# Performance work log

Hardware: AMD Instinct MI355X
Metric: run time of the kernel (lower is better)

The kernel has to match this reference:

```python
import math
import jax, jax.numpy as jnp
import numpy as np

B, T, D = 2, 2048, 2048
DH, NQ, NKV = 128, 16, 4
QPG = NQ // NKV  # queries per group = 4
ROPE_BASE = 10000.0
YARN_SCALE = 2.0
ORIG_MAX_LEN = 4096
BETA_FAST, BETA_SLOW = 32.0, 1.0
EPS = 1.1920929e-07  # torch.finfo(float32).eps, RMSNorm default
MSCALE = 0.1 * math.log(YARN_SCALE) + 1.0
ATTN_SCALE = 1.0 / (MSCALE * math.sqrt(DH))


def _yarn_inv_freq():
    inv_freq = 1.0 / ROPE_BASE ** (np.arange(0, DH, 2, dtype=np.float32) / DH)
    wavelengths = 2.0 * math.pi / inv_freq
    low_w = ORIG_MAX_LEN / BETA_SLOW
    high_w = ORIG_MAX_LEN / BETA_FAST
    gamma = np.clip((low_w - wavelengths) / (low_w - high_w), 0.0, 1.0)
    return (gamma * inv_freq + (1.0 - gamma) * inv_freq / YARN_SCALE).astype(np.float32)


def setup_inputs() -> dict:
    key = jax.random.key(0)
    k0, k1, k2, k3 = jax.random.split(key, 4)
    x = jax.random.normal(k0, (B, T, D), jnp.float32)
    Wq = jax.random.normal(k1, (D, DH * NQ), jnp.float32) * 0.02
    Wkv = jax.random.normal(k2, (D, 2 * DH * NKV), jnp.float32) * 0.02
    Wout = jax.random.normal(k3, (DH * NQ, D), jnp.float32) * 0.02
    q_norm_w = jnp.ones((DH,), jnp.float32)
    k_norm_w = jnp.ones((DH,), jnp.float32)
    inv_freq = jnp.asarray(_yarn_inv_freq())
    return {"x": x, "Wq": Wq, "Wkv": Wkv, "Wout": Wout,
            "q_norm_w": q_norm_w, "k_norm_w": k_norm_w, "inv_freq": inv_freq}


def _rmsnorm(x, w):
    ms = jnp.mean(jnp.square(x), axis=-1, keepdims=True)
    return x * jax.lax.rsqrt(ms + EPS) * w


def _apply_rope(x, inv_freq):
    # x: (..., T, DH)
    t = jnp.arange(x.shape[-2], dtype=inv_freq.dtype)
    freqs = jnp.outer(t, inv_freq)               # (T, DH//2)
    emb = jnp.concatenate([freqs, freqs], -1)     # (T, DH)
    cos, sin = jnp.cos(emb), jnp.sin(emb)
    half = x.shape[-1] // 2
    x_rot = jnp.concatenate([-x[..., half:], x[..., :half]], -1)
    return x * cos + x_rot * sin


def reference(x, Wq, Wkv, Wout, q_norm_w, k_norm_w, inv_freq):
    q = x @ Wq                                    # (B, T, NQ*DH)
    kv = x @ Wkv                                  # (B, T, 2*NKV*DH)
    k, v = jnp.split(kv, 2, axis=-1)              # each (B, T, NKV*DH)
    # b t (qpg g d) -> b qpg g t d
    q = q.reshape(B, T, QPG, NKV, DH).transpose(0, 2, 3, 1, 4)
    # b t (g d) -> b g t d
    k = k.reshape(B, T, NKV, DH).transpose(0, 2, 1, 3)
    v = v.reshape(B, T, NKV, DH).transpose(0, 2, 1, 3)
    q = _apply_rope(_rmsnorm(q, q_norm_w), inv_freq)
    k = _apply_rope(_rmsnorm(k, k_norm_w), inv_freq)
    scores = jnp.einsum('bqgtd,bgsd->bqgts', q, k) * ATTN_SCALE
    causal = jnp.tril(jnp.ones((T, T), bool))
    scores = jnp.where(causal, scores, -jnp.inf)
    attn = jax.nn.softmax(scores, axis=-1)
    out = jnp.einsum('bqgts,bgsd->bqgtd', attn, v)
    # b qpg g t d -> b t (qpg g d)
    out = out.transpose(0, 3, 1, 2, 4).reshape(B, T, NQ * DH)
    return out @ Wout
```

## Files before the change

kernel.cpp:

```cpp
#include <hip/hip_runtime.h>
#include <math.h>


typedef __attribute__((ext_vector_type(8))) short s16x8;
typedef __attribute__((ext_vector_type(4))) float f32x4;
typedef __attribute__((ext_vector_type(4))) unsigned int u32x4;

__device__ __forceinline__ unsigned short f2bf(float x) {
  union { float f; unsigned int u; } v; v.f = x;
  return (unsigned short)((v.u + 0x7FFFu + ((v.u >> 16) & 1u)) >> 16);
}

__device__ __forceinline__ float bf2f(unsigned short x) {
  union { unsigned int u; float f; } v; v.u = (unsigned int)x << 16;
  return v.f;
}

__device__ __forceinline__ unsigned int cvt_pk_bf16(float lo, float hi) {
  unsigned int r;
  asm("v_cvt_pk_bf16_f32 %0, %1, %2" : "=v"(r) : "v"(lo), "v"(hi));
  return r;
}

#define GLD_LDS16(g, l)                                            \
  __builtin_amdgcn_global_load_lds(                                \
      (const __attribute__((address_space(1))) void*)(g),          \
      (__attribute__((address_space(3))) void*)(l), 16, 0, 0)

__device__ __forceinline__ void wtrans_body(const float* __restrict__ in,
                                            unsigned short* __restrict__ out,
                                            int R, int C, int bx, int by,
                                            unsigned short lt[64][65]) {
  const int r0 = bx * 64, c0 = by * 64;
  const int j = threadIdx.x & 63, i4 = threadIdx.x >> 6;
#pragma unroll
  for (int p = 0; p < 16; ++p) {
    int i = p * 4 + i4;
    lt[i][j] = f2bf(in[(size_t)(r0 + i) * C + c0 + j]);
  }
  __syncthreads();
#pragma unroll
  for (int p = 0; p < 16; ++p) {
    int i = p * 4 + i4;
    out[(size_t)(c0 + i) * R + r0 + j] = lt[j][i];
  }
}

__global__ __launch_bounds__(256) void prep1_k(const float* __restrict__ x,
                                               const float* __restrict__ Wq,
                                               const float* __restrict__ Wkv,
                                               const float* __restrict__ Wout,
                                               const float* __restrict__ invf,
                                               unsigned short* __restrict__ xb,
                                               unsigned short* __restrict__ wqkvt,
                                               unsigned short* __restrict__ wot,
                                               float2* __restrict__ cstab) {
  __shared__ unsigned short lt[64][65];
  const int bid = blockIdx.x;
  if (bid < 8192) {
    int i = bid * 256 + threadIdx.x;
    float4 v = ((const float4*)x)[i];
    unsigned long long pack = (unsigned long long)f2bf(v.x)
                            | ((unsigned long long)f2bf(v.y) << 16)
                            | ((unsigned long long)f2bf(v.z) << 32)
                            | ((unsigned long long)f2bf(v.w) << 48);
    ((unsigned long long*)xb)[i] = pack;
  } else if (bid < 9216) {
    int b2 = bid - 8192;
    wtrans_body(Wq, wqkvt, 2048, 2048, b2 & 31, b2 >> 5, lt);
  } else if (bid < 9728) {
    int b2 = bid - 9216;
    wtrans_body(Wkv, wqkvt + (size_t)2048 * 2048, 2048, 1024, b2 & 31, b2 >> 5, lt);
  } else if (bid < 10752) {
    int b2 = bid - 9728;
    wtrans_body(Wout, wot, 2048, 2048, b2 & 31, b2 >> 5, lt);
  } else {
    int i = (bid - 10752) * 256 + threadIdx.x;
    int t = i >> 6, f = i & 63;
    float s, c;
    sincosf((float)t * invf[f], &s, &c);
    cstab[i] = make_float2(c, s);
  }
}

template <int OUTBF>
__global__ __launch_bounds__(256) void gemm_bt_t(const unsigned short* __restrict__ A,
                                                 const unsigned short* __restrict__ Bt,
                                                 void* __restrict__ Cv,
                                                 int M, int N, int K) {
  __shared__ alignas(16) unsigned short sA[2][128][32];
  __shared__ alignas(16) unsigned short sB[2][128][32];
  const int tid = threadIdx.x;
  const int lane = tid & 63;
  const int w = tid >> 6;
  const int wm = (w >> 1) * 64, wn = (w & 1) * 64;
  const int nwg = gridDim.x * gridDim.y;
  int bid = blockIdx.y * gridDim.x + blockIdx.x;
  bid = (bid & 7) * (nwg >> 3) + (bid >> 3);
  const int m0 = (bid % gridDim.x) * 128, n0 = (bid / gridDim.x) * 128;
  const int l15 = lane & 15, lhi = lane >> 4;
  f32x4 acc[4][4];
#pragma unroll
  for (int i = 0; i < 4; ++i)
#pragma unroll
    for (int j = 0; j < 4; ++j) acc[i][j] = (f32x4){0.f, 0.f, 0.f, 0.f};
  const int row = tid >> 2;
  const int srcslot = (tid & 3) ^ ((row >> 1) & 3);
  const unsigned short* gA0 = A + (size_t)(m0 + row) * K + srcslot * 8;
  const unsigned short* gA1 = A + (size_t)(m0 + 64 + row) * K + srcslot * 8;
  const unsigned short* gB0 = Bt + (size_t)(n0 + row) * K + srcslot * 8;
  const unsigned short* gB1 = Bt + (size_t)(n0 + 64 + row) * K + srcslot * 8;
  char* ldsA = (char*)&sA[0][0][0] + w * 1024;
  char* ldsB = (char*)&sB[0][0][0] + w * 1024;
  auto STAGE = [&](int bb, int k0) {
    GLD_LDS16(gA0 + k0, ldsA + bb * 8192);
    GLD_LDS16(gA1 + k0, ldsA + bb * 8192 + 4096);
    GLD_LDS16(gB0 + k0, ldsB + bb * 8192);
    GLD_LDS16(gB1 + k0, ldsB + bb * 8192 + 4096);
  };
  const int sphys = (lhi ^ ((l15 >> 1) & 3)) * 8;
  const int nt = K >> 5;
  STAGE(0, 0);
  __syncthreads();
  int cur = 0;
  for (int t = 0; t < nt; ++t) {
    if (t + 1 < nt) STAGE(cur ^ 1, (t + 1) * 32);
    s16x8 af[4], bfr[4];
#pragma unroll
    for (int i = 0; i < 4; ++i) af[i] = *(const s16x8*)&sA[cur][wm + i * 16 + l15][sphys];
#pragma unroll
    for (int j = 0; j < 4; ++j) bfr[j] = *(const s16x8*)&sB[cur][wn + j * 16 + l15][sphys];
#pragma unroll
    for (int i = 0; i < 4; ++i)
#pragma unroll
      for (int j = 0; j < 4; ++j)
        acc[i][j] = __builtin_amdgcn_mfma_f32_16x16x32_bf16(af[i], bfr[j], acc[i][j], 0, 0, 0);
    __syncthreads();
    cur ^= 1;
  }
  const int col0 = n0 + wn + l15;
  const int row00 = m0 + wm + lhi * 4;
  if (OUTBF) {
    unsigned short* C = (unsigned short*)Cv;
#pragma unroll
    for (int i = 0; i < 4; ++i)
#pragma unroll
      for (int j = 0; j < 4; ++j)
#pragma unroll
        for (int r = 0; r < 4; ++r)
          C[(size_t)(row00 + i * 16 + r) * N + col0 + j * 16] = f2bf(acc[i][j][r]);
  } else {
    float* C = (float*)Cv;
#pragma unroll
    for (int i = 0; i < 4; ++i)
#pragma unroll
      for (int j = 0; j < 4; ++j)
#pragma unroll
        for (int r = 0; r < 4; ++r)
          C[(size_t)(row00 + i * 16 + r) * N + col0 + j * 16] = acc[i][j][r];
  }
}

__global__ __launch_bounds__(256) void prep2_k(const unsigned short* __restrict__ qkvb,
                                               const float* __restrict__ qw,
                                               const float* __restrict__ kw,
                                               const float2* __restrict__ cstab,
                                               unsigned short* __restrict__ qT,
                                               unsigned short* __restrict__ kT,
                                               unsigned short* __restrict__ vT) {
  __shared__ unsigned short lt[64][65];
  const int bid = blockIdx.x;
  if (bid < 20480) {
    constexpr float FOLD =
        (float)(1.4426950408889634 / ((0.1 * 0.6931471805599453 + 1.0) * 11.313708498984761));
    int wid = bid * 4 + (threadIdx.x >> 6);
    int lane = threadIdx.x & 63;
    const unsigned short* src; const float* wgt; unsigned short* dst;
    int t; float fold;
    if (wid < 65536) {
      int bt = wid >> 4, h = wid & 15;
      int b = bt >> 11; t = bt & 2047;
      src = qkvb + (size_t)bt * 3072 + h * 128;
      wgt = qw;
      dst = qT + ((size_t)(b * 16 + h) * 2048 + t) * 128;
      fold = FOLD;
    } else {
      int id = wid - 65536;
      int bt = id >> 2, g = id & 3;
      int b = bt >> 11; t = bt & 2047;
      src = qkvb + (size_t)bt * 3072 + 2048 + g * 128;
      wgt = kw;
      dst = kT + ((size_t)(b * 4 + g) * 2048 + t) * 128;
      fold = 1.0f;
    }
    unsigned int vv = ((const unsigned int*)src)[lane];
    float vx = bf2f((unsigned short)(vv & 0xffff));
    float vy = bf2f((unsigned short)(vv >> 16));
    float ss = vx * vx + vy * vy;
#pragma unroll
    for (int m = 32; m; m >>= 1) ss += __shfl_xor(ss, m);
    float rs = rsqrtf(ss * (1.0f / 128.0f) + 1.1920929e-07f);
    float2 wv = ((const float2*)wgt)[lane];
    float xn0 = vx * rs * wv.x;
    float xn1 = vy * rs * wv.y;
    float px = __shfl_xor(xn0, 32);
    float py = __shfl_xor(xn1, 32);
    float sgn = (lane < 32) ? -1.0f : 1.0f;
    int f0 = (2 * lane) & 63;
    float4 cs = ((const float4*)cstab)[((size_t)t * 64 + f0) >> 1];
    float r0 = (xn0 * cs.x + sgn * px * cs.y) * fold;
    float r1 = (xn1 * cs.z + sgn * py * cs.w) * fold;
    unsigned int packed = (unsigned int)f2bf(r0) | ((unsigned int)f2bf(r1) << 16);
    ((unsigned int*)dst)[lane] = packed;
  } else {
    int b2 = bid - 20480;
    const int tt0 = (b2 & 31) * 64;
    const int dd0 = ((b2 >> 5) & 1) * 64;
    const int z = b2 >> 6;
    const int b = z >> 2, g = z & 3;
    const int j = threadIdx.x & 63, i4 = threadIdx.x >> 6;
    const unsigned short* src = qkvb + (size_t)b * 2048 * 3072 + 2560 + g * 128 + dd0;
#pragma unroll
    for (int p = 0; p < 16; ++p) {
      int i = p * 4 + i4;
      lt[i][j] = src[(size_t)(tt0 + i) * 3072 + j];
    }
    __syncthreads();
    unsigned short* dst = vT + ((size_t)(b * 4 + g) * 128 + dd0) * 2048 + tt0;
    const int jp = (j & 32) | (((j & 15) >> 2) << 3) | (((j >> 4) & 1) << 2) | (j & 3);
#pragma unroll
    for (int p = 0; p < 16; ++p) {
      int d = p * 4 + i4;
      dst[(size_t)d * 2048 + jp] = lt[j][d];
    }
  }
}

__global__ __launch_bounds__(256) void attn_k(const unsigned short* __restrict__ qT,
                                              const unsigned short* __restrict__ kT,
                                              const unsigned short* __restrict__ vT,
                                              unsigned short* __restrict__ ao) {
  __shared__ alignas(16) unsigned short sK[64][136];
  __shared__ alignas(16) unsigned short sVt[128][72];
  const int tid = threadIdx.x;
  const int lane = tid & 63;
  const int w = tid >> 6;
  const int l15 = lane & 15, lhi = lane >> 4;
  const int bid = blockIdx.x;
  const int xg = bid & 7;
  const int b = xg >> 2, g = xg & 3;
  const int hh = (bid >> 3) & 3;
  const int h = hh * 4 + g;
  const int qt = 31 - (bid >> 5);
  const int q0 = qt * 64;
  const unsigned short* Qb = qT + ((size_t)(b * 16 + h) * 2048) * 128;
  const unsigned short* Kb = kT + ((size_t)(b * 4 + g) * 2048) * 128;
  const unsigned short* Vb = vT + ((size_t)(b * 4 + g) * 128) * 2048;
  const int kr = tid >> 4, kc = (tid & 15) * 8;
  const int vr = tid >> 3, vc = (tid & 7) * 8;

  s16x8 qfr[4];
#pragma unroll
  for (int ks = 0; ks < 4; ++ks)
    qfr[ks] = *(const s16x8*)(Qb + (size_t)(q0 + w * 16 + l15) * 128 + ks * 32 + lhi * 8);

  u32x4 gk[4], gv[4];
#pragma unroll
  for (int p = 0; p < 4; ++p) {
    gk[p] = *(const u32x4*)(Kb + (size_t)(p * 16 + kr) * 128 + kc);
    gv[p] = *(const u32x4*)(Vb + (size_t)(p * 32 + vr) * 2048 + vc);
  }
  f32x4 o[8];
#pragma unroll
  for (int i = 0; i < 8; ++i) o[i] = (f32x4){0.f, 0.f, 0.f, 0.f};
  f32x4 o9 = (f32x4){0.f, 0.f, 0.f, 0.f};
  float m_run = -INFINITY;
  s16x8 ones;
#pragma unroll
  for (int j = 0; j < 8; ++j) ones[j] = (short)0x3F80;

  for (int kt = 0; kt <= qt; ++kt) {
    __syncthreads();
#pragma unroll
    for (int p = 0; p < 4; ++p) {
      *(u32x4*)&sK[p * 16 + kr][kc] = gk[p];
      *(u32x4*)&sVt[p * 32 + vr][vc] = gv[p];
    }
    __syncthreads();
    if (kt < qt) {
#pragma unroll
      for (int p = 0; p < 4; ++p) {
        gk[p] = *(const u32x4*)(Kb + (size_t)((kt + 1) * 64 + p * 16 + kr) * 128 + kc);
        gv[p] = *(const u32x4*)(Vb + (size_t)(p * 32 + vr) * 2048 + (kt + 1) * 64 + vc);
      }
    }
    f32x4 s[4];
#pragma unroll
    for (int jn = 0; jn < 4; ++jn) s[jn] = (f32x4){0.f, 0.f, 0.f, 0.f};
#pragma unroll
    for (int ks = 0; ks < 4; ++ks)
#pragma unroll
      for (int jn = 0; jn < 4; ++jn) {
        s16x8 ak = *(const s16x8*)&sK[jn * 16 + l15][ks * 32 + lhi * 8];
        s[jn] = __builtin_amdgcn_mfma_f32_16x16x32_bf16(ak, qfr[ks], s[jn], 0, 0, 0);
      }
    if (kt == qt) {
#pragma unroll
      for (int jn = 0; jn < 4; ++jn)
#pragma unroll
        for (int r = 0; r < 4; ++r)
          if (jn * 16 + lhi * 4 + r > w * 16 + l15) s[jn][r] = -INFINITY;
    }
    float mx = fmaxf(fmaxf(fmaxf(s[0][0], s[0][1]), fmaxf(s[0][2], s[0][3])),
                     fmaxf(fmaxf(s[1][0], s[1][1]), fmaxf(s[1][2], s[1][3])));
    mx = fmaxf(mx, fmaxf(fmaxf(fmaxf(s[2][0], s[2][1]), fmaxf(s[2][2], s[2][3])),
                         fmaxf(fmaxf(s[3][0], s[3][1]), fmaxf(s[3][2], s[3][3]))));
    mx = fmaxf(mx, __shfl_xor(mx, 16));
    mx = fmaxf(mx, __shfl_xor(mx, 32));
    if (!__all(mx - m_run <= 8.0f)) {
      float mnew = fmaxf(m_run, mx);
      float scale = exp2f(m_run - mnew);
      m_run = mnew;
      float sc_o[4];
#pragma unroll
      for (int r = 0; r < 4; ++r) sc_o[r] = __shfl(scale, lhi * 4 + r);
#pragma unroll
      for (int nt = 0; nt < 8; ++nt)
#pragma unroll
        for (int r = 0; r < 4; ++r) o[nt][r] *= sc_o[r];
#pragma unroll
      for (int r = 0; r < 4; ++r) o9[r] *= sc_o[r];
    }
    float pp[4][4];
#pragma unroll
    for (int jn = 0; jn < 4; ++jn)
#pragma unroll
      for (int r = 0; r < 4; ++r) pp[jn][r] = exp2f(s[jn][r] - m_run);
    union { s16x8 v; unsigned int d[4]; } pa0, pa1;
#pragma unroll
    for (int d = 0; d < 2; ++d) {
      pa0.d[d]     = cvt_pk_bf16(pp[0][2 * d], pp[0][2 * d + 1]);
      pa0.d[2 + d] = cvt_pk_bf16(pp[1][2 * d], pp[1][2 * d + 1]);
      pa1.d[d]     = cvt_pk_bf16(pp[2][2 * d], pp[2][2 * d + 1]);
      pa1.d[2 + d] = cvt_pk_bf16(pp[3][2 * d], pp[3][2 * d + 1]);
    }
    o9 = __builtin_amdgcn_mfma_f32_16x16x32_bf16(pa0.v, ones, o9, 0, 0, 0);
    o9 = __builtin_amdgcn_mfma_f32_16x16x32_bf16(pa1.v, ones, o9, 0, 0, 0);
#pragma unroll
    for (int nt = 0; nt < 8; ++nt) {
      s16x8 vb0 = *(const s16x8*)&sVt[nt * 16 + l15][lhi * 8];
      o[nt] = __builtin_amdgcn_mfma_f32_16x16x32_bf16(pa0.v, vb0, o[nt], 0, 0, 0);
    }
#pragma unroll
    for (int nt = 0; nt < 8; ++nt) {
      s16x8 vb1 = *(const s16x8*)&sVt[nt * 16 + l15][32 + lhi * 8];
      o[nt] = __builtin_amdgcn_mfma_f32_16x16x32_bf16(pa1.v, vb1, o[nt], 0, 0, 0);
    }
  }
#pragma unroll
  for (int r = 0; r < 4; ++r) {
    float invr = 1.0f / o9[r];
    int t = q0 + w * 16 + lhi * 4 + r;
    size_t base = ((size_t)b * 2048 + t) * 2048 + h * 128;
#pragma unroll
    for (int nt = 0; nt < 8; ++nt)
      ao[base + nt * 16 + l15] = f2bf(o[nt][r] * invr);
  }
}

extern "C" void kernel_launch(void* const* d_in, const int* in_sizes, int n_in,
                              void* d_out, int out_size, void* d_ws, size_t ws_size,
                              hipStream_t stream) {
  (void)in_sizes; (void)n_in; (void)out_size; (void)ws_size;
  const float* x    = (const float*)d_in[0];
  const float* Wq   = (const float*)d_in[1];
  const float* Wkv  = (const float*)d_in[2];
  const float* Wout = (const float*)d_in[3];
  const float* qw   = (const float*)d_in[4];
  const float* kw   = (const float*)d_in[5];
  const float* invf = (const float*)d_in[6];
  float* out = (float*)d_out;

  char* ws = (char*)d_ws;
  size_t off = 0;
  auto alloc = [&](size_t bytes) -> void* {
    void* p = ws + off; off += (bytes + 255) & ~(size_t)255; return p;
  };
  unsigned short* xb    = (unsigned short*)alloc((size_t)4096 * 2048 * 2);
  unsigned short* wqkvt = (unsigned short*)alloc((size_t)3072 * 2048 * 2);
  unsigned short* wot   = (unsigned short*)alloc((size_t)2048 * 2048 * 2);
  unsigned short* qkvb  = (unsigned short*)alloc((size_t)4096 * 3072 * 2);
  float2* cstab = (float2*)alloc((size_t)2048 * 64 * 8);
  unsigned short* qT = (unsigned short*)alloc((size_t)2 * 16 * 2048 * 128 * 2);
  unsigned short* kT = (unsigned short*)alloc((size_t)2 * 4 * 2048 * 128 * 2);
  unsigned short* vT = (unsigned short*)alloc((size_t)2 * 4 * 128 * 2048 * 2);
  unsigned short* ao = (unsigned short*)alloc((size_t)4096 * 2048 * 2);

  prep1_k<<<11264, 256, 0, stream>>>(x, Wq, Wkv, Wout, invf, xb, wqkvt, wot, cstab);
  gemm_bt_t<1><<<dim3(32, 24), 256, 0, stream>>>(xb, wqkvt, qkvb, 4096, 3072, 2048);
  prep2_k<<<20992, 256, 0, stream>>>(qkvb, qw, kw, cstab, qT, kT, vT);
  attn_k<<<1024, 256, 0, stream>>>(qT, kT, vT, ao);
  gemm_bt_t<0><<<dim3(32, 16), 256, 0, stream>>>(ao, wot, out, 4096, 2048, 2048);
}
```

Before: 212.4 us.

## Double-buffer attention K/V tiles via direct global-to-LDS loads with XOR swizzle

The attention kernel now stages K and V tiles straight from global memory into LDS using the GLD_LDS16 direct-load path, with two LDS buffers so the next tile loads while the current one is computed. This removes the register staging round trip and one barrier per iteration. The padded LDS rows are replaced by an XOR swizzle on 16-byte chunks to avoid bank conflicts. LDS use roughly doubles, which may lower occupancy, and the per-iteration vmcnt(0) wait still serialises on the prefetch issued in the previous iteration.

```diff
diff --git a/kernel.cpp b/kernel.cpp
--- a/kernel.cpp
+++ b/kernel.cpp
@@ -240,12 +240,13 @@
                                               const unsigned short* __restrict__ kT,
                                               const unsigned short* __restrict__ vT,
                                               unsigned short* __restrict__ ao) {
-  __shared__ alignas(16) unsigned short sK[64][136];
-  __shared__ alignas(16) unsigned short sVt[128][72];
+  __shared__ alignas(16) unsigned short sK2[2][64][128];
+  __shared__ alignas(16) unsigned short sV2[2][128][64];
   const int tid = threadIdx.x;
   const int lane = tid & 63;
   const int w = tid >> 6;
   const int l15 = lane & 15, lhi = lane >> 4;
+  const int l8 = lane >> 3;
   const int bid = blockIdx.x;
   const int xg = bid & 7;
   const int b = xg >> 2, g = xg & 3;
@@ -256,20 +257,27 @@
   const unsigned short* Qb = qT + ((size_t)(b * 16 + h) * 2048) * 128;
   const unsigned short* Kb = kT + ((size_t)(b * 4 + g) * 2048) * 128;
   const unsigned short* Vb = vT + ((size_t)(b * 4 + g) * 128) * 2048;
-  const int kr = tid >> 4, kc = (tid & 15) * 8;
-  const int vr = tid >> 3, vc = (tid & 7) * 8;
 
   s16x8 qfr[4];
 #pragma unroll
   for (int ks = 0; ks < 4; ++ks)
     qfr[ks] = *(const s16x8*)(Qb + (size_t)(q0 + w * 16 + l15) * 128 + ks * 32 + lhi * 8);
 
-  u32x4 gk[4], gv[4];
-#pragma unroll
-  for (int p = 0; p < 4; ++p) {
-    gk[p] = *(const u32x4*)(Kb + (size_t)(p * 16 + kr) * 128 + kc);
-    gv[p] = *(const u32x4*)(Vb + (size_t)(p * 32 + vr) * 2048 + vc);
-  }
+  const int sgK = l15 ^ ((w * 4 + lhi) & 7);
+  const int sgV = (lane & 7) ^ (l8 & 7);
+  char* ldsK = (char*)&sK2[0][0][0] + w * 1024;
+  char* ldsV = (char*)&sV2[0][0][0] + w * 1024;
+  auto STAGEKV = [&](int bb, int kt) {
+#pragma unroll
+    for (int p = 0; p < 4; ++p) {
+      GLD_LDS16(Kb + (size_t)(kt * 64 + p * 16 + w * 4 + lhi) * 128 + sgK * 8,
+                ldsK + bb * 16384 + p * 4096);
+      GLD_LDS16(Vb + (size_t)(p * 32 + w * 8 + l8) * 2048 + kt * 64 + sgV * 8,
+                ldsV + bb * 16384 + p * 4096);
+    }
+  };
+  const int xr = l15 & 7;
+
   f32x4 o[8];
 #pragma unroll
   for (int i = 0; i < 8; ++i) o[i] = (f32x4){0.f, 0.f, 0.f, 0.f};
@@ -279,21 +287,12 @@
 #pragma unroll
   for (int j = 0; j < 8; ++j) ones[j] = (short)0x3F80;
 
+  STAGEKV(0, 0);
+  int cur = 0;
   for (int kt = 0; kt <= qt; ++kt) {
+    asm volatile("s_waitcnt vmcnt(0)" ::: "memory");
     __syncthreads();
-#pragma unroll
-    for (int p = 0; p < 4; ++p) {
-      *(u32x4*)&sK[p * 16 + kr][kc] = gk[p];
-      *(u32x4*)&sVt[p * 32 + vr][vc] = gv[p];
-    }
-    __syncthreads();
-    if (kt < qt) {
-#pragma unroll
-      for (int p = 0; p < 4; ++p) {
-        gk[p] = *(const u32x4*)(Kb + (size_t)((kt + 1) * 64 + p * 16 + kr) * 128 + kc);
-        gv[p] = *(const u32x4*)(Vb + (size_t)(p * 32 + vr) * 2048 + (kt + 1) * 64 + vc);
-      }
-    }
+    if (kt < qt) STAGEKV(cur ^ 1, kt + 1);
     f32x4 s[4];
 #pragma unroll
     for (int jn = 0; jn < 4; ++jn) s[jn] = (f32x4){0.f, 0.f, 0.f, 0.f};
@@ -301,7 +300,7 @@
     for (int ks = 0; ks < 4; ++ks)
 #pragma unroll
       for (int jn = 0; jn < 4; ++jn) {
-        s16x8 ak = *(const s16x8*)&sK[jn * 16 + l15][ks * 32 + lhi * 8];
+        s16x8 ak = *(const s16x8*)&sK2[cur][jn * 16 + l15][((ks * 4 + lhi) ^ xr) * 8];
         s[jn] = __builtin_amdgcn_mfma_f32_16x16x32_bf16(ak, qfr[ks], s[jn], 0, 0, 0);
       }
     if (kt == qt) {
@@ -348,14 +347,15 @@
     o9 = __builtin_amdgcn_mfma_f32_16x16x32_bf16(pa1.v, ones, o9, 0, 0, 0);
 #pragma unroll
     for (int nt = 0; nt < 8; ++nt) {
-      s16x8 vb0 = *(const s16x8*)&sVt[nt * 16 + l15][lhi * 8];
+      s16x8 vb0 = *(const s16x8*)&sV2[cur][nt * 16 + l15][(lhi ^ xr) * 8];
       o[nt] = __builtin_amdgcn_mfma_f32_16x16x32_bf16(pa0.v, vb0, o[nt], 0, 0, 0);
     }
 #pragma unroll
     for (int nt = 0; nt < 8; ++nt) {
-      s16x8 vb1 = *(const s16x8*)&sVt[nt * 16 + l15][32 + lhi * 8];
+      s16x8 vb1 = *(const s16x8*)&sV2[cur][nt * 16 + l15][((lhi + 4) ^ xr) * 8];
       o[nt] = __builtin_amdgcn_mfma_f32_16x16x32_bf16(pa1.v, vb1, o[nt], 0, 0, 0);
     }
+    cur ^= 1;
   }
 #pragma unroll
   for (int r = 0; r < 4; ++r) {
```

Result: faster. 201.8 us (-5.0%).
